# Kernel tuning notes

Hardware: AMD Instinct MI355X
Metric: run time of the kernel (lower is better)

## Reference

```python
import jax, jax.numpy as jnp
import numpy as np

HIDDEN = 512
B, H, W = 8, 48, 48
SCALE = 1.0 / np.sqrt(HIDDEN).astype(np.float32)


def conv1x1(x, w, b):
    # x: [B, C, H, W], w: [O, C], b: [O]  (1x1 Conv2d == channel matmul)
    return jnp.einsum('bchw,oc->bohw', x, w) + b[None, :, None, None]


def setup_inputs() -> dict:
    key = jax.random.key(0)
    ks = jax.random.split(key, 10)
    s = 1.0 / np.sqrt(HIDDEN)
    return {
        'locx': jax.random.normal(ks[0], (B, HIDDEN, H, W), dtype=jnp.float32),
        'glox': jax.random.normal(ks[1], (B, HIDDEN, H, W), dtype=jnp.float32),
        'Wq': jax.random.normal(ks[2], (HIDDEN, HIDDEN), dtype=jnp.float32) * s,
        'bq': jax.random.normal(ks[3], (HIDDEN,), dtype=jnp.float32) * 0.01,
        'Wk': jax.random.normal(ks[4], (HIDDEN, HIDDEN), dtype=jnp.float32) * s,
        'bk': jax.random.normal(ks[5], (HIDDEN,), dtype=jnp.float32) * 0.01,
        'Wv': jax.random.normal(ks[6], (HIDDEN, HIDDEN), dtype=jnp.float32) * s,
        'bv': jax.random.normal(ks[7], (HIDDEN,), dtype=jnp.float32) * 0.01,
        'Wo': jax.random.normal(ks[8], (HIDDEN, HIDDEN), dtype=jnp.float32) * s,
        'bo': jax.random.normal(ks[9], (HIDDEN,), dtype=jnp.float32) * 0.01,
    }


def reference(locx, glox, Wq, bq, Wk, bk, Wv, bv, Wo, bo):
    b, c, h, w = locx.shape
    # 1x1 conv projections
    q = conv1x1(locx, Wq, bq).reshape(b, c, h * w)   # [B, C, N]
    k = conv1x1(glox, Wk, bk).reshape(b, c, -1)      # [B, C, M]
    v = conv1x1(glox, Wv, bv).reshape(b, c, -1)      # [B, C, M]
    # scores = Q^T K / sqrt(hidden)  -> [B, N, M]
    scores = jnp.einsum('bcn,bcm->bnm', q, k) * SCALE
    probs = jax.nn.softmax(scores, axis=-1)           # dropout rate 0.0 -> identity
    # context = probs @ V^T -> [B, N, C] -> [B, C, H, H]
    ctx = jnp.einsum('bnm,bcm->bcn', probs, v).reshape(b, c, h, h)
    out = conv1x1(ctx, Wo, bo)                        # proj dropout 0.0 -> identity
    return out
```

## Files before the change

### kernel.cpp

```cpp
#include <hip/hip_runtime.h>
#include <hip/hip_bf16.h>

typedef __attribute__((ext_vector_type(4))) float f32x4;
typedef __attribute__((ext_vector_type(8))) short bf16x8;
typedef __attribute__((ext_vector_type(4))) short s16x4;

#define C_DIM 512
#define N_PIX 2304
#define N_BATCH 8
#define ATT_SCALE 0.04419417382415922f
#define NJB 9

typedef __attribute__((address_space(3))) unsigned int lds_u32;
typedef const __attribute__((address_space(1))) unsigned int glob_u32;

__device__ __forceinline__ void gl2lds16(const __hip_bfloat16* g, __hip_bfloat16* l)
{
    __builtin_amdgcn_global_load_lds((glob_u32*)g, (lds_u32*)l, 16, 0, 0);
}

#define GBAR() __builtin_amdgcn_s_barrier()
#define GVM0() asm volatile("s_waitcnt vmcnt(0)" ::: "memory")



#define BAR()  __builtin_amdgcn_s_barrier()
#define LGK0() asm volatile("s_waitcnt lgkmcnt(0)" ::: "memory")
#define VM4()  asm volatile("s_waitcnt vmcnt(4)" ::: "memory")
#define VM0()  asm volatile("s_waitcnt vmcnt(0)" ::: "memory")
#define PRIO(p) __builtin_amdgcn_s_setprio(p)

#define STAGE_A(dd, hh, tk) do { \
    _Pragma("unroll") \
    for (int ss = 0; ss < 2; ++ss) { \
        const int ur0 = wave * 16 + ss * 8; \
        const int row0 = ((ur0 >> 6) << 7) + (hh) * 64 + (ur0 & 63); \
        gl2lds16(gA + (size_t)row0 * C_DIM + (tk) * 64, \
                 (__hip_bfloat16*)&LA[dd][row0 * 64]); \
    } } while (0)

#define STAGE_B(dd, bb, tk) do { \
    _Pragma("unroll") \
    for (int ss = 0; ss < 2; ++ss) { \
        const int ur0 = wave * 16 + ss * 8; \
        const int row0 = ((ur0 >> 5) << 6) + (bb) * 32 + (ur0 & 31); \
        gl2lds16(gB + (size_t)row0 * C_DIM + (tk) * 64, \
                 (__hip_bfloat16*)&LB[dd][row0 * 64]); \
    } } while (0)

#define LOAD_A(dd, hh) do { \
    _Pragma("unroll") \
    for (int tt = 0; tt < 4; ++tt) { \
        const int rb = (wr * 128 + (hh) * 64 + tt * 16 + fr) * 64; \
        _Pragma("unroll") \
        for (int kk = 0; kk < 2; ++kk) \
            aF[tt][kk] = *(const bf16x8*)(&LA[dd][rb + (((kk * 4 + fq) ^ sw) << 3)]); \
    } } while (0)

#define LOAD_B(dd, bb, dst) do { \
    _Pragma("unroll") \
    for (int s2 = 0; s2 < 2; ++s2) { \
        const int rb = (wc * 64 + (bb) * 32 + s2 * 16 + fr) * 64; \
        _Pragma("unroll") \
        for (int kk = 0; kk < 2; ++kk) \
            dst[s2][kk] = *(const bf16x8*)(&LB[dd][rb + (((kk * 4 + fq) ^ sw) << 3)]); \
    } } while (0)

#define MFMA_Q(HH, BB, bsrc) do { \
    _Pragma("unroll") \
    for (int tt = 0; tt < 4; ++tt) \
    _Pragma("unroll") \
    for (int s2 = 0; s2 < 2; ++s2) \
    _Pragma("unroll") \
    for (int kk = 0; kk < 2; ++kk) \
        acc[(HH) * 4 + tt][(BB) * 2 + s2] = __builtin_amdgcn_mfma_f32_16x16x32_bf16( \
            aF[tt][kk], bsrc[s2][kk], acc[(HH) * 4 + tt][(BB) * 2 + s2], 0, 0, 0); \
    } while (0)

template<int NS>
__global__ __launch_bounds__(512, 2)
void s_only(const __hip_bfloat16* __restrict__ Tm, const __hip_bfloat16* __restrict__ Xgt,
            __hip_bfloat16* __restrict__ Pu, float* __restrict__ rp,
            const float* __restrict__ vvec, int bz_off, long sPu)
{
    __shared__ __hip_bfloat16 LA[2][256 * 64];
    __shared__ __hip_bfloat16 LB[2][256 * 64];

    const int lin = blockIdx.x;
    const int bz  = lin % NS + bz_off;
    const int t   = lin / NS;
    const int ib  = t / 9;
    const int jb  = t % 9;
    const long sQ = (long)N_PIX * C_DIM;

    const __hip_bfloat16* A = Tm  + (size_t)bz * sQ;
    const __hip_bfloat16* B = Xgt + (size_t)bz * sQ;
    __hip_bfloat16* D = Pu + (size_t)bz * (size_t)sPu;

    const int i0 = ib * 256;
    const int j0 = jb * 256;

    const int tid  = threadIdx.x;
    const int lane = tid & 63;
    const int wave = tid >> 6;

    const int lrow = lane >> 3;
    const int lcs  = (lane & 7) ^ lrow;
    const __hip_bfloat16* gA = A + (size_t)(i0 + lrow) * C_DIM + lcs * 8;
    const __hip_bfloat16* gB = B + (size_t)(j0 + lrow) * C_DIM + lcs * 8;

    const int fr = lane & 15;
    const int fq = lane >> 4;
    const int sw = fr & 7;
    const int wr = wave >> 2;
    const int wc = wave & 3;

    f32x4 acc[8][4];
#pragma unroll
    for (int a = 0; a < 8; ++a)
#pragma unroll
        for (int b = 0; b < 4; ++b)
            acc[a][b] = (f32x4){0.f, 0.f, 0.f, 0.f};

    bf16x8 aF[4][2], bF0[2][2], bF1[2][2];

    STAGE_A(0, 0, 0); STAGE_B(0, 0, 0); STAGE_B(0, 1, 0); STAGE_A(0, 1, 0);
    STAGE_A(1, 0, 1); STAGE_B(1, 1, 1);
    VM4();
    BAR();

    for (int kt = 0; kt < 6; ++kt) {
        const int d = kt & 1, e = d ^ 1;
        LOAD_A(d, 0); LOAD_B(d, 0, bF0);
        STAGE_A(e, 1, kt + 1);
        BAR(); LGK0();
        PRIO(1); MFMA_Q(0, 0, bF0); PRIO(0);
        BAR();
        LOAD_B(d, 1, bF1);
        STAGE_B(e, 0, kt + 1);
        BAR(); LGK0();
        PRIO(1); MFMA_Q(0, 1, bF1); PRIO(0);
        BAR();
        LOAD_A(d, 1);
        STAGE_A(d, 0, kt + 2);
        BAR(); LGK0();
        PRIO(1); MFMA_Q(1, 1, bF1); PRIO(0);
        BAR();
        STAGE_B(d, 1, kt + 2);
        VM4();
        BAR();
        PRIO(1); MFMA_Q(1, 0, bF0); PRIO(0);
        BAR();
    }
    {
        LOAD_A(0, 0); LOAD_B(0, 0, bF0);
        STAGE_A(1, 1, 7);
        BAR(); LGK0();
        PRIO(1); MFMA_Q(0, 0, bF0); PRIO(0);
        BAR();
        LOAD_B(0, 1, bF1);
        STAGE_B(1, 0, 7);
        BAR(); LGK0();
        PRIO(1); MFMA_Q(0, 1, bF1); PRIO(0);
        BAR();
        LOAD_A(0, 1);
        BAR(); LGK0();
        PRIO(1); MFMA_Q(1, 1, bF1); PRIO(0);
        BAR();
        VM0();
        BAR();
        PRIO(1); MFMA_Q(1, 0, bF0); PRIO(0);
        BAR();
    }
    {
        LOAD_A(1, 0); LOAD_B(1, 0, bF0);
        BAR(); LGK0();
        PRIO(1); MFMA_Q(0, 0, bF0); PRIO(0);
        BAR();
        LOAD_B(1, 1, bF1);
        BAR(); LGK0();
        PRIO(1); MFMA_Q(0, 1, bF1); PRIO(0);
        BAR();
        LOAD_A(1, 1);
        BAR(); LGK0();
        PRIO(1); MFMA_Q(1, 1, bF1); PRIO(0);
        BAR();
        PRIO(1); MFMA_Q(1, 0, bF0); PRIO(0);
    }

    float vb[4];
#pragma unroll
    for (int b = 0; b < 4; ++b)
        vb[b] = vvec[(size_t)bz * N_PIX + j0 + wc * 64 + b * 16 + fr];

    float rpart[8][4];
#pragma unroll
    for (int a = 0; a < 8; ++a)
#pragma unroll
        for (int r = 0; r < 4; ++r)
            rpart[a][r] = 0.f;
#pragma unroll
    for (int a = 0; a < 8; ++a) {
        const int grow = i0 + wr * 128 + a * 16 + fq * 4;
#pragma unroll
        for (int b = 0; b < 4; ++b) {
            const int col = j0 + wc * 64 + b * 16 + fr;
#pragma unroll
            for (int r = 0; r < 4; ++r) {
                float v = __expf(ATT_SCALE * (acc[a][b][r] + vb[b]));
                rpart[a][r] += v;
                D[(size_t)(grow + r) * N_PIX + col] = __float2bfloat16(v);
            }
        }
    }
#pragma unroll
    for (int m = 1; m < 16; m <<= 1)
#pragma unroll
        for (int a = 0; a < 8; ++a)
#pragma unroll
            for (int r = 0; r < 4; ++r)
                rpart[a][r] += __shfl_xor(rpart[a][r], m);
    float* rsl = (float*)&LA[0][0];
    __syncthreads();
    if (fr == 0) {
#pragma unroll
        for (int a = 0; a < 8; ++a)
#pragma unroll
            for (int r = 0; r < 4; ++r)
                rsl[wave * 128 + a * 16 + fq * 4 + r] = rpart[a][r];
    }
    __syncthreads();
    if (tid < 256) {
        const int wr2 = tid >> 7, rl = tid & 127;
        float s = rsl[(wr2 * 4 + 0) * 128 + rl] + rsl[(wr2 * 4 + 1) * 128 + rl]
                + rsl[(wr2 * 4 + 2) * 128 + rl] + rsl[(wr2 * 4 + 3) * 128 + rl];
        rp[((size_t)jb * N_BATCH + bz) * N_PIX + i0 + tid] = s;
    }
}

#undef STAGE_A
#undef STAGE_B
#undef LOAD_A
#undef LOAD_B
#undef MFMA_Q
#undef BAR
#undef LGK0
#undef VM4
#undef VM0
#undef PRIO


#define PV_STAGE(ee, tk) do { \
    _Pragma("unroll") \
    for (int ss = 0; ss < 2; ++ss) \
        gl2lds16(ga + (size_t)ss * 8 * N_PIX + (tk) * 64, \
                 laA + (ee) * (64 * 64) + ss * 8 * 64); \
    _Pragma("unroll") \
    for (int ss = 0; ss < 4; ++ss) \
        gl2lds16(gb + (size_t)ss * 8 * N_PIX + (tk) * 64, \
                 laB + (ee) * (128 * 64) + ss * 8 * 64); \
    } while (0)

#define PV_COMP(dd) do { \
    _Pragma("unroll") \
    for (int kk = 0; kk < 2; ++kk) { \
        bf16x8 af[2], bfr[4]; \
        const int ca = ((kk * 4 + fq) ^ sw) << 3; \
        _Pragma("unroll") \
        for (int tt = 0; tt < 2; ++tt) \
            af[tt]  = *(const bf16x8*)(&As[dd][(wi + tt * 16 + fr) * 64 + ca]); \
        _Pragma("unroll") \
        for (int tt = 0; tt < 4; ++tt) \
            bfr[tt] = *(const bf16x8*)(&Bs[dd][(wj + tt * 16 + fr) * 64 + ca]); \
        _Pragma("unroll") \
        for (int a = 0; a < 2; ++a) \
        _Pragma("unroll") \
        for (int b = 0; b < 4; ++b) \
            acc[a][b] = __builtin_amdgcn_mfma_f32_16x16x32_bf16( \
                af[a], bfr[b], acc[a][b], 0, 0, 0); \
    } } while (0)

template<int NS>
__global__ __launch_bounds__(256)
void pv_out(const __hip_bfloat16* __restrict__ Vp, const __hip_bfloat16* __restrict__ Pu,
            float* __restrict__ out, const float* __restrict__ bo,
            const float* __restrict__ rp, int bz_off, long sPu)
{
    __shared__ __hip_bfloat16 As[2][64 * 64];
    __shared__ __hip_bfloat16 Bs[2][128 * 64];

    const int lin = blockIdx.x;
    const int bz  = lin % NS + bz_off;
    const int t   = lin / NS;
    const int ib  = t % 8;
    const int jb  = t / 8;
    const int i0  = ib * 64;
    const int j0  = jb * 128;

    const long sCN = (long)C_DIM * N_PIX;
    const __hip_bfloat16* A = Vp + (size_t)bz * sCN;
    const __hip_bfloat16* B = Pu + (size_t)bz * (size_t)sPu;
    float* D = out + (size_t)bz * sCN;

    const int tid  = threadIdx.x;
    const int lane = tid & 63;
    const int wave = tid >> 6;

    const int lrow = lane >> 3;
    const int lcs  = (lane & 7) ^ lrow;
    const __hip_bfloat16* ga = A + (size_t)(i0 + wave * 16 + lrow) * N_PIX + lcs * 8;
    const __hip_bfloat16* gb = B + (size_t)(j0 + wave * 32 + lrow) * N_PIX + lcs * 8;
    __hip_bfloat16* laA = &As[0][wave * 16 * 64];
    __hip_bfloat16* laB = &Bs[0][wave * 32 * 64];

    const int fr = lane & 15;
    const int fq = lane >> 4;
    const int sw = fr & 7;
    const int wi = (wave >> 1) * 32;
    const int wj = (wave & 1) * 64;

    f32x4 acc[2][4];
#pragma unroll
    for (int a = 0; a < 2; ++a)
#pragma unroll
        for (int b = 0; b < 4; ++b)
            acc[a][b] = (f32x4){0.f, 0.f, 0.f, 0.f};

    PV_STAGE(0, 0);
    GVM0(); GBAR();

#pragma unroll 1
    for (int kt = 0; kt < 34; kt += 2) {
        PV_STAGE(1, kt + 1);
        PV_COMP(0);
        GVM0(); GBAR();
        PV_STAGE(0, kt + 2);
        PV_COMP(1);
        GVM0(); GBAR();
    }
    PV_STAGE(1, 35);
    PV_COMP(0);
    GVM0(); GBAR();
    PV_COMP(1);

    const int orow = fq * 4;
    float rjv[4];
#pragma unroll
    for (int b = 0; b < 4; ++b) {
        int j = j0 + wj + b * 16 + fr;
        float s = 0.f;
#pragma unroll
        for (int jj = 0; jj < NJB; ++jj)
            s += rp[((size_t)jj * N_BATCH + bz) * N_PIX + j];
        rjv[b] = 1.f / s;
    }

#pragma unroll
    for (int a = 0; a < 2; ++a) {
        int ibx = i0 + wi + a * 16 + orow;
#pragma unroll
        for (int r = 0; r < 4; ++r) {
            float bi = bo[ibx + r];
#pragma unroll
            for (int b = 0; b < 4; ++b) {
                int j = j0 + wj + b * 16 + fr;
                D[(size_t)(ibx + r) * N_PIX + j] = acc[a][b][r] * rjv[b] + bi;
            }
        }
    }
}

#undef PV_STAGE
#undef PV_COMP


#define PJ_STAGE(ee, tk) do { \
    _Pragma("unroll") \
    for (int ss = 0; ss < 4; ++ss) { \
        gl2lds16(ga + (size_t)ss * 8 * C_DIM + (tk) * 64, \
                 laA + (ee) * (128 * 64) + ss * 8 * 64); \
        gl2lds16(gb + (size_t)ss * 8 * C_DIM + (tk) * 64, \
                 laB + (ee) * (128 * 64) + ss * 8 * 64); \
    } } while (0)

#define PJ_COMP(dd) do { \
    _Pragma("unroll") \
    for (int kk = 0; kk < 2; ++kk) { \
        bf16x8 af[4], bfr[4]; \
        const int ca = ((kk * 4 + fq) ^ sw) << 3; \
        _Pragma("unroll") \
        for (int tt = 0; tt < 4; ++tt) { \
            af[tt]  = *(const bf16x8*)(&As[dd][(wi + tt * 16 + fr) * 64 + ca]); \
            bfr[tt] = *(const bf16x8*)(&Bs[dd][(wj + tt * 16 + fr) * 64 + ca]); \
        } \
        _Pragma("unroll") \
        for (int a = 0; a < 4; ++a) \
        _Pragma("unroll") \
        for (int b = 0; b < 4; ++b) \
            acc[a][b] = __builtin_amdgcn_mfma_f32_16x16x32_bf16( \
                af[a], bfr[b], acc[a][b], 0, 0, 0); \
    } } while (0)

#define PJ_LOOP() do { \
    PJ_STAGE(0, 0); \
    GVM0(); GBAR(); \
    _Pragma("unroll 1") \
    for (int kt = 0; kt < 6; kt += 2) { \
        PJ_STAGE(1, kt + 1); \
        PJ_COMP(0); \
        GVM0(); GBAR(); \
        PJ_STAGE(0, kt + 2); \
        PJ_COMP(1); \
        GVM0(); GBAR(); \
    } \
    PJ_STAGE(1, 7); \
    PJ_COMP(0); \
    GVM0(); GBAR(); \
    PJ_COMP(1); \
    } while (0)

__global__ __launch_bounds__(256)
void proj2(const __hip_bfloat16* __restrict__ Xlt,
           const __hip_bfloat16* __restrict__ Xgt,
           const __hip_bfloat16* __restrict__ matT,
           const __hip_bfloat16* __restrict__ Wov,
           const float* __restrict__ bovp,
           __hip_bfloat16* __restrict__ Tm,
           __hip_bfloat16* __restrict__ Vp)
{
    __shared__ __hip_bfloat16 As[2][128 * 64];
    __shared__ __hip_bfloat16 Bs[2][128 * 64];

    const int lin = blockIdx.x;
    const int s   = lin % 16;
    const int bz  = s & 7;
    const int m2  = s >> 3;
    const int t2  = lin / 16;
    const int j0  = (t2 & 3) * 128;
    const int i0  = (t2 >> 2) * 128;
    const long sNC = (long)N_PIX * C_DIM;

    const __hip_bfloat16* Ab = (m2 ? Xgt : Xlt) + (size_t)bz * sNC;
    const __hip_bfloat16* Bb = m2 ? Wov : matT;

    const int tid  = threadIdx.x;
    const int lane = tid & 63;
    const int wave = tid >> 6;

    const int lrow = lane >> 3;
    const int lcs  = (lane & 7) ^ lrow;
    const __hip_bfloat16* ga = Ab + (size_t)(i0 + wave * 32 + lrow) * C_DIM + lcs * 8;
    const __hip_bfloat16* gb = Bb + (size_t)(j0 + wave * 32 + lrow) * C_DIM + lcs * 8;
    __hip_bfloat16* laA = &As[0][wave * 32 * 64];
    __hip_bfloat16* laB = &Bs[0][wave * 32 * 64];

    const int fr = lane & 15;
    const int fq = lane >> 4;
    const int sw = fr & 7;
    const int wi = (wave >> 1) * 64;
    const int wj = (wave & 1) * 64;

    f32x4 acc[4][4];
#pragma unroll
    for (int a = 0; a < 4; ++a)
#pragma unroll
        for (int b = 0; b < 4; ++b)
            acc[a][b] = (f32x4){0.f, 0.f, 0.f, 0.f};

    PJ_LOOP();

    const int orow = fq * 4;
    if (m2 == 0) {
        __hip_bfloat16* D = Tm + (size_t)bz * sNC;
#pragma unroll
        for (int a = 0; a < 4; ++a) {
            int ibx = i0 + wi + a * 16 + orow;
#pragma unroll
            for (int b = 0; b < 4; ++b) {
                int j = j0 + wj + b * 16 + fr;
#pragma unroll
                for (int r = 0; r < 4; ++r)
                    D[(size_t)(ibx + r) * C_DIM + j] = __float2bfloat16(acc[a][b][r]);
            }
        }
    } else {
        __hip_bfloat16* Dvp = Vp + (size_t)bz * sNC;
        float bvb[4];
#pragma unroll
        for (int b = 0; b < 4; ++b)
            bvb[b] = bovp[j0 + wj + b * 16 + fr];
        __syncthreads();
        __hip_bfloat16* Tt = (__hip_bfloat16*)&As[0][0];
#pragma unroll
        for (int h = 0; h < 2; ++h) {
            if ((wave & 1) == h) {
#pragma unroll
                for (int a = 0; a < 4; ++a) {
                    int rl = wi + a * 16 + orow;
#pragma unroll
                    for (int b = 0; b < 4; ++b) {
                        int cl = b * 16 + fr;
#pragma unroll
                        for (int r = 0; r < 4; ++r)
                            Tt[(rl + r) * 65 + cl] =
                                __float2bfloat16(acc[a][b][r] + bvb[b]);
                    }
                }
            }
            __syncthreads();
            {
                const int lj = tid >> 2, ic = (tid & 3) * 32;
                union { __hip_bfloat16 h8[32]; int4 v4[4]; } u;
#pragma unroll
                for (int q = 0; q < 32; ++q)
                    u.h8[q] = Tt[(ic + q) * 65 + lj];
                __hip_bfloat16* dst = Dvp + (size_t)(j0 + h * 64 + lj) * N_PIX + i0 + ic;
#pragma unroll
                for (int q4 = 0; q4 < 4; ++q4)
                    ((int4*)dst)[q4] = u.v4[q4];
            }
            __syncthreads();
        }
    }
}

__global__ __launch_bounds__(256)
void wmix(const __hip_bfloat16* __restrict__ WkT, const __hip_bfloat16* __restrict__ WqT,
          const __hip_bfloat16* __restrict__ wo_bf, const __hip_bfloat16* __restrict__ WvT,
          __hip_bfloat16* __restrict__ matT, __hip_bfloat16* __restrict__ Wov,
          const __hip_bfloat16* __restrict__ Xgt, const float* __restrict__ wvbuf,
          float* __restrict__ vvec)
{
    __shared__ __hip_bfloat16 As[2][128 * 64];
    __shared__ __hip_bfloat16 Bs[2][128 * 64];

    const int lin = blockIdx.x;
    const int tid = threadIdx.x;

    if (lin >= 32) {
        float* wvs = (float*)&As[0][0];
        wvs[tid] = wvbuf[tid];
        wvs[tid + 256] = wvbuf[tid + 256];
        __syncthreads();
        const int blk = lin - 32;
        const int b   = blk / 9;
        const int m0  = (blk % 9) * 256;
        const __hip_bfloat16* row = Xgt + ((size_t)b * N_PIX + m0 + tid) * C_DIM;
        float acc = 0.f;
#pragma unroll 4
        for (int c8 = 0; c8 < 64; ++c8) {
            union { bf16x8 v; __hip_bfloat16 h[8]; } u;
            u.v = *(const bf16x8*)(row + c8 * 8);
#pragma unroll
            for (int j = 0; j < 8; ++j)
                acc += __bfloat162float(u.h[j]) * wvs[c8 * 8 + j];
        }
        vvec[(size_t)b * N_PIX + m0 + tid] = acc;
        return;
    }

    const int m2 = lin >> 4;
    const int t2 = lin & 15;
    const int j0 = (t2 & 3) * 128;
    const int i0 = (t2 >> 2) * 128;

    const __hip_bfloat16* Ab = m2 ? wo_bf : WkT;
    const __hip_bfloat16* Bb = m2 ? WvT   : WqT;
    __hip_bfloat16* D = m2 ? Wov : matT;

    const int lane = tid & 63;
    const int wave = tid >> 6;
    const int lrow = lane >> 3;
    const int lcs  = (lane & 7) ^ lrow;
    const __hip_bfloat16* ga = Ab + (size_t)(i0 + wave * 32 + lrow) * C_DIM + lcs * 8;
    const __hip_bfloat16* gb = Bb + (size_t)(j0 + wave * 32 + lrow) * C_DIM + lcs * 8;
    __hip_bfloat16* laA = &As[0][wave * 32 * 64];
    __hip_bfloat16* laB = &Bs[0][wave * 32 * 64];

    const int fr = lane & 15;
    const int fq = lane >> 4;
    const int sw = fr & 7;
    const int wi = (wave >> 1) * 64;
    const int wj = (wave & 1) * 64;

    f32x4 acc[4][4];
#pragma unroll
    for (int a = 0; a < 4; ++a)
#pragma unroll
        for (int b = 0; b < 4; ++b)
            acc[a][b] = (f32x4){0.f, 0.f, 0.f, 0.f};

    PJ_LOOP();

    const int orow = fq * 4;
#pragma unroll
    for (int a = 0; a < 4; ++a) {
        int ibx = i0 + wi + a * 16 + orow;
#pragma unroll
        for (int b = 0; b < 4; ++b) {
            int j = j0 + wj + b * 16 + fr;
#pragma unroll
            for (int r = 0; r < 4; ++r)
                D[(size_t)(ibx + r) * C_DIM + j] = __float2bfloat16(acc[a][b][r]);
        }
    }
}

#undef PJ_STAGE
#undef PJ_COMP
#undef PJ_LOOP

__global__ __launch_bounds__(256)
void prep(const float* __restrict__ locx, const float* __restrict__ glox,
          __hip_bfloat16* __restrict__ Xlt, __hip_bfloat16* __restrict__ Xgt,
          const float* __restrict__ Wq, const float* __restrict__ Wk,
          const float* __restrict__ Wv, const float* __restrict__ Wo,
          __hip_bfloat16* __restrict__ wo_bf,
          __hip_bfloat16* __restrict__ WqT, __hip_bfloat16* __restrict__ WkT,
          __hip_bfloat16* __restrict__ WvT,
          const float* __restrict__ bq, const float* __restrict__ bv,
          float* __restrict__ wvbuf, float* __restrict__ bovbuf)
{
    __shared__ float t[64 * 65];
    const int lin = blockIdx.x;
    const int tid = threadIdx.x;

    if (lin < 4608) {
        const int z  = lin & 15;
        const int t2 = lin >> 4;
        const int c0 = (t2 & 7) * 64;
        const int n0 = (t2 >> 3) * 64;
        const size_t b = z & 7;
        const float* Xb = ((z < 8) ? locx : glox) + b * (size_t)C_DIM * N_PIX;
        __hip_bfloat16* Xt = (z < 8) ? Xlt : Xgt;

        const int n_l = tid & 63;
        const int c_b = tid >> 6;
#pragma unroll
        for (int s = 0; s < 16; ++s) {
            int c_l = c_b + s * 4;
            t[c_l * 65 + n_l] = Xb[(size_t)(c0 + c_l) * N_PIX + n0 + n_l];
        }
        __syncthreads();

        const int cc = (tid & 7) * 8;
        const int nb = tid >> 3;
#pragma unroll
        for (int it = 0; it < 2; ++it) {
            int n2 = nb + it * 32;
            union { __hip_bfloat16 h[8]; int4 v; } u;
#pragma unroll
            for (int w = 0; w < 8; ++w)
                u.h[w] = __float2bfloat16(t[(cc + w) * 65 + n2]);
            *(int4*)(&Xt[(b * N_PIX + n0 + n2) * C_DIM + c0 + cc]) = u.v;
        }
    } else if (lin < 4864) {
        const int idx = lin - 4608;
        const int i = (idx * 256 + tid) * 4;
        float4 f = *(const float4*)(Wo + i);
        union { __hip_bfloat16 h[4]; s16x4 q; } u;
        u.h[0] = __float2bfloat16(f.x);
        u.h[1] = __float2bfloat16(f.y);
        u.h[2] = __float2bfloat16(f.z);
        u.h[3] = __float2bfloat16(f.w);
        *(s16x4*)(wo_bf + i) = u.q;
    } else if (lin < 5056) {
        const int widx = lin - 4864;
        const int w    = widx >> 6;
        const int tile = widx & 63;
        const float* S = (w == 0) ? Wq : (w == 1) ? Wk : Wv;
        __hip_bfloat16* Dt = (w == 0) ? WqT : (w == 1) ? WkT : WvT;
        const int o0  = (tile & 7) * 64;
        const int c0t = (tile >> 3) * 64;

        const int n_l = tid & 63;
        const int c_b = tid >> 6;
#pragma unroll
        for (int s = 0; s < 16; ++s) {
            int o_l = c_b + s * 4;
            t[o_l * 65 + n_l] = S[(size_t)(o0 + o_l) * 512 + c0t + n_l];
        }
        __syncthreads();

        const int cc = (tid & 7) * 8;
        const int nb = tid >> 3;
#pragma unroll
        for (int it = 0; it < 2; ++it) {
            int c_r = nb + it * 32;
            union { __hip_bfloat16 h[8]; int4 v; } u;
#pragma unroll
            for (int w8 = 0; w8 < 8; ++w8)
                u.h[w8] = __float2bfloat16(t[(cc + w8) * 65 + c_r]);
            *(int4*)(&Dt[(size_t)(c0t + c_r) * 512 + o0 + cc]) = u.v;
        }
    } else if (lin == 5056) {
        float a0 = 0.f, a1 = 0.f;
        for (int o = 0; o < 512; ++o) {
            float bb = bq[o];
            a0 += Wk[(size_t)o * 512 + tid] * bb;
            a1 += Wk[(size_t)o * 512 + tid + 256] * bb;
        }
        wvbuf[tid] = a0;
        wvbuf[tid + 256] = a1;
    } else {
#pragma unroll
        for (int half = 0; half < 2; ++half) {
            int o = tid + half * 256;
            float acc = 0.f;
            for (int c4 = 0; c4 < 128; ++c4) {
                float4 f = *(const float4*)(Wo + (size_t)o * 512 + c4 * 4);
                float4 g = *(const float4*)(bv + c4 * 4);
                acc += f.x * g.x + f.y * g.y + f.z * g.z + f.w * g.w;
            }
            bovbuf[o] = acc;
        }
    }
}

extern "C" void kernel_launch(void* const* d_in, const int* in_sizes, int n_in,
                              void* d_out, int out_size, void* d_ws, size_t ws_size,
                              hipStream_t stream)
{
    const float* locx = (const float*)d_in[0];
    const float* glox = (const float*)d_in[1];
    const float* Wq = (const float*)d_in[2];
    const float* bq = (const float*)d_in[3];
    const float* Wk = (const float*)d_in[4];
    const float* bk = (const float*)d_in[5];
    const float* Wv = (const float*)d_in[6];
    const float* bv = (const float*)d_in[7];
    const float* Wo = (const float*)d_in[8];
    const float* bo = (const float*)d_in[9];
    float* out = (float*)d_out;
    (void)bk;

    const int C = C_DIM, N = N_PIX;
    const size_t WB   = (size_t)C * C * 2;
    const size_t szX  = (size_t)N_BATCH * N * C * 2;
    const size_t szP1 = (size_t)N * N * 2;
    const size_t szRP = (size_t)NJB * N_BATCH * N * 4;
    const size_t szV  = (size_t)N_BATCH * N * 4;

    char* ws = (char*)d_ws;
    size_t off = 0;
    auto alloc = [&](size_t bytes) {
        char* p = ws + off;
        off += (bytes + 255) & ~(size_t)255;
        return p;
    };
    __hip_bfloat16* wo_bf = (__hip_bfloat16*)alloc(WB);
    __hip_bfloat16* WqT   = (__hip_bfloat16*)alloc(WB);
    __hip_bfloat16* WkT   = (__hip_bfloat16*)alloc(WB);
    __hip_bfloat16* WvT   = (__hip_bfloat16*)alloc(WB);
    __hip_bfloat16* matT  = (__hip_bfloat16*)alloc(WB);
    __hip_bfloat16* Wov   = (__hip_bfloat16*)alloc(WB);
    float*          wvb   = (float*)alloc(512 * 4);
    float*          bovb  = (float*)alloc(512 * 4);
    float*          vvec  = (float*)alloc(szV);
    __hip_bfloat16* Xlt   = (__hip_bfloat16*)alloc(szX);
    __hip_bfloat16* Xgt   = (__hip_bfloat16*)alloc(szX);
    __hip_bfloat16* Tm    = (__hip_bfloat16*)alloc(szX);
    __hip_bfloat16* Vp    = (__hip_bfloat16*)alloc(szX);
    float*          rp    = (float*)alloc(szRP);
    const size_t fixed = off;
    bool full = (ws_size >= fixed + 8 * szP1 + 4096);
    __hip_bfloat16* Pu = (__hip_bfloat16*)alloc(full ? 8 * szP1 : szP1);

    const dim3 blk(256);

    prep<<<dim3(5058), blk, 0, stream>>>(locx, glox, Xlt, Xgt,
                                         Wq, Wk, Wv, Wo, wo_bf, WqT, WkT, WvT,
                                         bq, bv, wvb, bovb);
    wmix<<<dim3(104), blk, 0, stream>>>(WkT, WqT, wo_bf, WvT, matT, Wov,
                                        Xgt, wvb, vvec);
    proj2<<<dim3(16 * 72), blk, 0, stream>>>(Xlt, Xgt, matT, Wov, bovb, Tm, Vp);

    if (full) {
        s_only<8><<<dim3(8 * 81), dim3(512), 0, stream>>>(
            Tm, Xgt, Pu, rp, vvec, 0, (long)N * N);
        pv_out<8><<<dim3(8 * 144), blk, 0, stream>>>(
            Vp, Pu, out, bo, rp, 0, (long)N * N);
    } else {
        for (int r = 0; r < N_BATCH; ++r) {
            s_only<1><<<dim3(81), dim3(512), 0, stream>>>(
                Tm, Xgt, Pu, rp, vvec, r, 0);
            pv_out<1><<<dim3(144), blk, 0, stream>>>(
                Vp, Pu, out, bo, rp, r, 0);
        }
    }
}
```

Measured before the change: 359.9 us.

## Merge weight prep into single kernel and enlarge PV output tile to 128x128

The separate weight-transpose/convert pass and the wmix kernel are folded into one prep kernel. It computes the Wk^T·Wq and Wo·Wv mixes directly from fp32 weights converted on the fly into LDS, and computes vvec directly from glox. This removes one launch and the intermediate bf16 transposed weight buffers. Separately, pv_out's tile grows from 64x128 to 128x128 with 4x4 MFMA accumulators per wave, which halves the block count and the redundant reloads of the P matrix, at the cost of more registers and LDS per block.

```diff
diff --git a/kernel.cpp b/kernel.cpp
--- a/kernel.cpp
+++ b/kernel.cpp
@@ -252,28 +252,25 @@
 
 #define PV_STAGE(ee, tk) do { \
     _Pragma("unroll") \
-    for (int ss = 0; ss < 2; ++ss) \
+    for (int ss = 0; ss < 4; ++ss) { \
         gl2lds16(ga + (size_t)ss * 8 * N_PIX + (tk) * 64, \
-                 laA + (ee) * (64 * 64) + ss * 8 * 64); \
-    _Pragma("unroll") \
-    for (int ss = 0; ss < 4; ++ss) \
+                 laA + (ee) * (128 * 64) + ss * 8 * 64); \
         gl2lds16(gb + (size_t)ss * 8 * N_PIX + (tk) * 64, \
                  laB + (ee) * (128 * 64) + ss * 8 * 64); \
-    } while (0)
+    } } while (0)
 
 #define PV_COMP(dd) do { \
     _Pragma("unroll") \
     for (int kk = 0; kk < 2; ++kk) { \
-        bf16x8 af[2], bfr[4]; \
+        bf16x8 af[4], bfr[4]; \
         const int ca = ((kk * 4 + fq) ^ sw) << 3; \
         _Pragma("unroll") \
-        for (int tt = 0; tt < 2; ++tt) \
+        for (int tt = 0; tt < 4; ++tt) { \
             af[tt]  = *(const bf16x8*)(&As[dd][(wi + tt * 16 + fr) * 64 + ca]); \
+            bfr[tt] = *(const bf16x8*)(&Bs[dd][(wj + tt * 16 + fr) * 64 + ca]); \
+        } \
         _Pragma("unroll") \
-        for (int tt = 0; tt < 4; ++tt) \
-            bfr[tt] = *(const bf16x8*)(&Bs[dd][(wj + tt * 16 + fr) * 64 + ca]); \
-        _Pragma("unroll") \
-        for (int a = 0; a < 2; ++a) \
+        for (int a = 0; a < 4; ++a) \
         _Pragma("unroll") \
         for (int b = 0; b < 4; ++b) \
             acc[a][b] = __builtin_amdgcn_mfma_f32_16x16x32_bf16( \
@@ -286,15 +283,15 @@
             float* __restrict__ out, const float* __restrict__ bo,
             const float* __restrict__ rp, int bz_off, long sPu)
 {
-    __shared__ __hip_bfloat16 As[2][64 * 64];
+    __shared__ __hip_bfloat16 As[2][128 * 64];
     __shared__ __hip_bfloat16 Bs[2][128 * 64];
 
     const int lin = blockIdx.x;
     const int bz  = lin % NS + bz_off;
     const int t   = lin / NS;
-    const int ib  = t % 8;
-    const int jb  = t / 8;
-    const int i0  = ib * 64;
+    const int ib  = t % 4;
+    const int jb  = t / 4;
+    const int i0  = ib * 128;
     const int j0  = jb * 128;
 
     const long sCN = (long)C_DIM * N_PIX;
@@ -308,20 +305,20 @@
 
     const int lrow = lane >> 3;
     const int lcs  = (lane & 7) ^ lrow;
-    const __hip_bfloat16* ga = A + (size_t)(i0 + wave * 16 + lrow) * N_PIX + lcs * 8;
+    const __hip_bfloat16* ga = A + (size_t)(i0 + wave * 32 + lrow) * N_PIX + lcs * 8;
     const __hip_bfloat16* gb = B + (size_t)(j0 + wave * 32 + lrow) * N_PIX + lcs * 8;
-    __hip_bfloat16* laA = &As[0][wave * 16 * 64];
+    __hip_bfloat16* laA = &As[0][wave * 32 * 64];
     __hip_bfloat16* laB = &Bs[0][wave * 32 * 64];
 
     const int fr = lane & 15;
     const int fq = lane >> 4;
     const int sw = fr & 7;
-    const int wi = (wave >> 1) * 32;
+    const int wi = (wave >> 1) * 64;
     const int wj = (wave & 1) * 64;
 
-    f32x4 acc[2][4];
-#pragma unroll
-    for (int a = 0; a < 2; ++a)
+    f32x4 acc[4][4];
+#pragma unroll
+    for (int a = 0; a < 4; ++a)
 #pragma unroll
         for (int b = 0; b < 4; ++b)
             acc[a][b] = (f32x4){0.f, 0.f, 0.f, 0.f};
@@ -356,7 +353,7 @@
     }
 
 #pragma unroll
-    for (int a = 0; a < 2; ++a) {
+    for (int a = 0; a < 4; ++a) {
         int ibx = i0 + wi + a * 16 + orow;
 #pragma unroll
         for (int r = 0; r < 4; ++r) {
@@ -524,185 +521,151 @@
     }
 }
 
+#undef PJ_STAGE
+#undef PJ_COMP
+#undef PJ_LOOP
+
 __global__ __launch_bounds__(256)
-void wmix(const __hip_bfloat16* __restrict__ WkT, const __hip_bfloat16* __restrict__ WqT,
-          const __hip_bfloat16* __restrict__ wo_bf, const __hip_bfloat16* __restrict__ WvT,
+void prep(const float* __restrict__ locx, const float* __restrict__ glox,
+          const float* __restrict__ Wq, const float* __restrict__ Wk,
+          const float* __restrict__ Wv, const float* __restrict__ Wo,
+          const float* __restrict__ bq, const float* __restrict__ bv,
+          __hip_bfloat16* __restrict__ Xlt, __hip_bfloat16* __restrict__ Xgt,
           __hip_bfloat16* __restrict__ matT, __hip_bfloat16* __restrict__ Wov,
-          const __hip_bfloat16* __restrict__ Xgt, const float* __restrict__ wvbuf,
-          float* __restrict__ vvec)
+          float* __restrict__ vvec, float* __restrict__ bovbuf)
 {
-    __shared__ __hip_bfloat16 As[2][128 * 64];
-    __shared__ __hip_bfloat16 Bs[2][128 * 64];
-
+    __shared__ __align__(16) char shm[16640];
     const int lin = blockIdx.x;
     const int tid = threadIdx.x;
 
-    if (lin >= 32) {
-        float* wvs = (float*)&As[0][0];
-        wvs[tid] = wvbuf[tid];
-        wvs[tid + 256] = wvbuf[tid + 256];
-        __syncthreads();
+    if (lin < 32) {
+        __hip_bfloat16* As = (__hip_bfloat16*)shm;
+        __hip_bfloat16* Bs = (__hip_bfloat16*)(shm + 8192);
+        const int m2 = lin >> 4;
+        const int t2 = lin & 15;
+        const int j0 = (t2 & 3) * 128;
+        const int i0 = (t2 >> 2) * 128;
+
+        const int lane = tid & 63;
+        const int wave = tid >> 6;
+        const int fr = lane & 15;
+        const int fq = lane >> 4;
+        const int sw2 = fr & 3;
+        const int wi = (wave >> 1) * 64;
+        const int wj = (wave & 1) * 64;
+
+        f32x4 acc[4][4];
+#pragma unroll
+        for (int a = 0; a < 4; ++a)
+#pragma unroll
+            for (int b = 0; b < 4; ++b)
+                acc[a][b] = (f32x4){0.f, 0.f, 0.f, 0.f};
+
+        const float* SB = m2 ? Wv : Wq;
+        const int o_r = tid >> 3;
+        const int cc0 = (tid & 7) * 16;
+
+#pragma unroll 1
+        for (int o0 = 0; o0 < 512; o0 += 32) {
+            if (m2 == 0) {
+                const float* src = Wk + (size_t)(o0 + o_r) * 512 + i0 + cc0;
+                float v[16];
+#pragma unroll
+                for (int q4 = 0; q4 < 4; ++q4) {
+                    float4 f = *(const float4*)(src + q4 * 4);
+                    v[q4 * 4 + 0] = f.x; v[q4 * 4 + 1] = f.y;
+                    v[q4 * 4 + 2] = f.z; v[q4 * 4 + 3] = f.w;
+                }
+#pragma unroll
+                for (int q = 0; q < 16; ++q) {
+                    const int col = cc0 + q;
+                    const int byt = col * 64 + ((((o_r >> 3) ^ (col & 3)) << 4))
+                                  + (o_r & 7) * 2;
+                    *(__hip_bfloat16*)((char*)As + byt) = __float2bfloat16(v[q]);
+                }
+            } else {
+                const int r = tid >> 1;
+#pragma unroll
+                for (int s = 0; s < 2; ++s) {
+                    const int cp = (tid & 1) * 2 + s;
+                    const float* src = Wo + (size_t)(i0 + r) * 512 + o0 + cp * 8;
+                    float4 f0 = *(const float4*)(src);
+                    float4 f1 = *(const float4*)(src + 4);
+                    union { __hip_bfloat16 h[8]; int4 v4; } u;
+                    u.h[0] = __float2bfloat16(f0.x); u.h[1] = __float2bfloat16(f0.y);
+                    u.h[2] = __float2bfloat16(f0.z); u.h[3] = __float2bfloat16(f0.w);
+                    u.h[4] = __float2bfloat16(f1.x); u.h[5] = __float2bfloat16(f1.y);
+                    u.h[6] = __float2bfloat16(f1.z); u.h[7] = __float2bfloat16(f1.w);
+                    *(int4*)(As + r * 32 + ((cp ^ (r & 3)) << 3)) = u.v4;
+                }
+            }
+            {
+                const float* src = SB + (size_t)(o0 + o_r) * 512 + j0 + cc0;
+                float v[16];
+#pragma unroll
+                for (int q4 = 0; q4 < 4; ++q4) {
+                    float4 f = *(const float4*)(src + q4 * 4);
+                    v[q4 * 4 + 0] = f.x; v[q4 * 4 + 1] = f.y;
+                    v[q4 * 4 + 2] = f.z; v[q4 * 4 + 3] = f.w;
+                }
+#pragma unroll
+                for (int q = 0; q < 16; ++q) {
+                    const int col = cc0 + q;
+                    const int byt = col * 64 + ((((o_r >> 3) ^ (col & 3)) << 4))
+                                  + (o_r & 7) * 2;
+                    *(__hip_bfloat16*)((char*)Bs + byt) = __float2bfloat16(v[q]);
+                }
+            }
+            __syncthreads();
+            bf16x8 af[4], bfm[4];
+#pragma unroll
+            for (int tt = 0; tt < 4; ++tt) {
+                af[tt]  = *(const bf16x8*)(As + (wi + tt * 16 + fr) * 32
+                                              + ((fq ^ sw2) << 3));
+                bfm[tt] = *(const bf16x8*)(Bs + (wj + tt * 16 + fr) * 32
+                                              + ((fq ^ sw2) << 3));
+            }
+#pragma unroll
+            for (int a = 0; a < 4; ++a)
+#pragma unroll
+                for (int b = 0; b < 4; ++b)
+                    acc[a][b] = __builtin_amdgcn_mfma_f32_16x16x32_bf16(
+                        af[a], bfm[b], acc[a][b], 0, 0, 0);
+            __syncthreads();
+        }
+        __hip_bfloat16* D = m2 ? Wov : matT;
+        const int orow = fq * 4;
+#pragma unroll
+        for (int a = 0; a < 4; ++a) {
+            int ibx = i0 + wi + a * 16 + orow;
+#pragma unroll
+            for (int b = 0; b < 4; ++b) {
+                int j = j0 + wj + b * 16 + fr;
+#pragma unroll
+                for (int r = 0; r < 4; ++r)
+                    D[(size_t)(ibx + r) * 512 + j] = __float2bfloat16(acc[a][b][r]);
+            }
+        }
+    } else if (lin < 104) {
         const int blk = lin - 32;
         const int b   = blk / 9;
         const int m0  = (blk % 9) * 256;
-        const __hip_bfloat16* row = Xgt + ((size_t)b * N_PIX + m0 + tid) * C_DIM;
-        float acc = 0.f;
-#pragma unroll 4
-        for (int c8 = 0; c8 < 64; ++c8) {
-            union { bf16x8 v; __hip_bfloat16 h[8]; } u;
-            u.v = *(const bf16x8*)(row + c8 * 8);
-#pragma unroll
-            for (int j = 0; j < 8; ++j)
-                acc += __bfloat162float(u.h[j]) * wvs[c8 * 8 + j];
-        }
-        vvec[(size_t)b * N_PIX + m0 + tid] = acc;
-        return;
-    }
-
-    const int m2 = lin >> 4;
-    const int t2 = lin & 15;
-    const int j0 = (t2 & 3) * 128;
-    const int i0 = (t2 >> 2) * 128;
-
-    const __hip_bfloat16* Ab = m2 ? wo_bf : WkT;
-    const __hip_bfloat16* Bb = m2 ? WvT   : WqT;
-    __hip_bfloat16* D = m2 ? Wov : matT;
-
-    const int lane = tid & 63;
-    const int wave = tid >> 6;
-    const int lrow = lane >> 3;
-    const int lcs  = (lane & 7) ^ lrow;
-    const __hip_bfloat16* ga = Ab + (size_t)(i0 + wave * 32 + lrow) * C_DIM + lcs * 8;
-    const __hip_bfloat16* gb = Bb + (size_t)(j0 + wave * 32 + lrow) * C_DIM + lcs * 8;
-    __hip_bfloat16* laA = &As[0][wave * 32 * 64];
-    __hip_bfloat16* laB = &Bs[0][wave * 32 * 64];
-
-    const int fr = lane & 15;
-    const int fq = lane >> 4;
-    const int sw = fr & 7;
-    const int wi = (wave >> 1) * 64;
-    const int wj = (wave & 1) * 64;
-
-    f32x4 acc[4][4];
-#pragma unroll
-    for (int a = 0; a < 4; ++a)
-#pragma unroll
-        for (int b = 0; b < 4; ++b)
-            acc[a][b] = (f32x4){0.f, 0.f, 0.f, 0.f};
-
-    PJ_LOOP();
-
-    const int orow = fq * 4;
-#pragma unroll
-    for (int a = 0; a < 4; ++a) {
-        int ibx = i0 + wi + a * 16 + orow;
-#pragma unroll
-        for (int b = 0; b < 4; ++b) {
-            int j = j0 + wj + b * 16 + fr;
-#pragma unroll
-            for (int r = 0; r < 4; ++r)
-                D[(size_t)(ibx + r) * C_DIM + j] = __float2bfloat16(acc[a][b][r]);
-        }
-    }
-}
-
-#undef PJ_STAGE
-#undef PJ_COMP
-#undef PJ_LOOP
-
-__global__ __launch_bounds__(256)
-void prep(const float* __restrict__ locx, const float* __restrict__ glox,
-          __hip_bfloat16* __restrict__ Xlt, __hip_bfloat16* __restrict__ Xgt,
-          const float* __restrict__ Wq, const float* __restrict__ Wk,
-          const float* __restrict__ Wv, const float* __restrict__ Wo,
-          __hip_bfloat16* __restrict__ wo_bf,
-          __hip_bfloat16* __restrict__ WqT, __hip_bfloat16* __restrict__ WkT,
-          __hip_bfloat16* __restrict__ WvT,
-          const float* __restrict__ bq, const float* __restrict__ bv,
-          float* __restrict__ wvbuf, float* __restrict__ bovbuf)
-{
-    __shared__ float t[64 * 65];
-    const int lin = blockIdx.x;
-    const int tid = threadIdx.x;
-
-    if (lin < 4608) {
-        const int z  = lin & 15;
-        const int t2 = lin >> 4;
-        const int c0 = (t2 & 7) * 64;
-        const int n0 = (t2 >> 3) * 64;
-        const size_t b = z & 7;
-        const float* Xb = ((z < 8) ? locx : glox) + b * (size_t)C_DIM * N_PIX;
-        __hip_bfloat16* Xt = (z < 8) ? Xlt : Xgt;
-
-        const int n_l = tid & 63;
-        const int c_b = tid >> 6;
-#pragma unroll
-        for (int s = 0; s < 16; ++s) {
-            int c_l = c_b + s * 4;
-            t[c_l * 65 + n_l] = Xb[(size_t)(c0 + c_l) * N_PIX + n0 + n_l];
-        }
-        __syncthreads();
-
-        const int cc = (tid & 7) * 8;
-        const int nb = tid >> 3;
-#pragma unroll
-        for (int it = 0; it < 2; ++it) {
-            int n2 = nb + it * 32;
-            union { __hip_bfloat16 h[8]; int4 v; } u;
-#pragma unroll
-            for (int w = 0; w < 8; ++w)
-                u.h[w] = __float2bfloat16(t[(cc + w) * 65 + n2]);
-            *(int4*)(&Xt[(b * N_PIX + n0 + n2) * C_DIM + c0 + cc]) = u.v;
-        }
-    } else if (lin < 4864) {
-        const int idx = lin - 4608;
-        const int i = (idx * 256 + tid) * 4;
-        float4 f = *(const float4*)(Wo + i);
-        union { __hip_bfloat16 h[4]; s16x4 q; } u;
-        u.h[0] = __float2bfloat16(f.x);
-        u.h[1] = __float2bfloat16(f.y);
-        u.h[2] = __float2bfloat16(f.z);
-        u.h[3] = __float2bfloat16(f.w);
-        *(s16x4*)(wo_bf + i) = u.q;
-    } else if (lin < 5056) {
-        const int widx = lin - 4864;
-        const int w    = widx >> 6;
-        const int tile = widx & 63;
-        const float* S = (w == 0) ? Wq : (w == 1) ? Wk : Wv;
-        __hip_bfloat16* Dt = (w == 0) ? WqT : (w == 1) ? WkT : WvT;
-        const int o0  = (tile & 7) * 64;
-        const int c0t = (tile >> 3) * 64;
-
-        const int n_l = tid & 63;
-        const int c_b = tid >> 6;
-#pragma unroll
-        for (int s = 0; s < 16; ++s) {
-            int o_l = c_b + s * 4;
-            t[o_l * 65 + n_l] = S[(size_t)(o0 + o_l) * 512 + c0t + n_l];
-        }
-        __syncthreads();
-
-        const int cc = (tid & 7) * 8;
-        const int nb = tid >> 3;
-#pragma unroll
-        for (int it = 0; it < 2; ++it) {
-            int c_r = nb + it * 32;
-            union { __hip_bfloat16 h[8]; int4 v; } u;
-#pragma unroll
-            for (int w8 = 0; w8 < 8; ++w8)
-                u.h[w8] = __float2bfloat16(t[(cc + w8) * 65 + c_r]);
-            *(int4*)(&Dt[(size_t)(c0t + c_r) * 512 + o0 + cc]) = u.v;
-        }
-    } else if (lin == 5056) {
         float a0 = 0.f, a1 = 0.f;
         for (int o = 0; o < 512; ++o) {
-            float bb = bq[o];
+            const float bb = bq[o];
             a0 += Wk[(size_t)o * 512 + tid] * bb;
             a1 += Wk[(size_t)o * 512 + tid + 256] * bb;
         }
-        wvbuf[tid] = a0;
-        wvbuf[tid + 256] = a1;
-    } else {
+        float* wvs = (float*)shm;
+        wvs[tid] = a0;
+        wvs[tid + 256] = a1;
+        __syncthreads();
+        const float* col = glox + (size_t)b * 512 * N_PIX + m0 + tid;
+        float acc = 0.f;
+        for (int c = 0; c < 512; ++c)
+            acc += col[(size_t)c * N_PIX] * wvs[c];
+        vvec[(size_t)b * N_PIX + m0 + tid] = acc;
+    } else if (lin == 104) {
 #pragma unroll
         for (int half = 0; half < 2; ++half) {
             int o = tid + half * 256;
@@ -713,6 +676,37 @@
                 acc += f.x * g.x + f.y * g.y + f.z * g.z + f.w * g.w;
             }
             bovbuf[o] = acc;
+        }
+    } else {
+        float* t = (float*)shm;
+        const int lin2 = lin - 105;
+        const int z  = lin2 & 15;
+        const int t2 = lin2 >> 4;
+        const int c0 = (t2 & 7) * 64;
+        const int n0 = (t2 >> 3) * 64;
+        const size_t b = z & 7;
+        const float* Xb = ((z < 8) ? locx : glox) + b * (size_t)C_DIM * N_PIX;
+        __hip_bfloat16* Xt = (z < 8) ? Xlt : Xgt;
+
+        const int n_l = tid & 63;
+        const int c_b = tid >> 6;
+#pragma unroll
+        for (int s = 0; s < 16; ++s) {
+            int c_l = c_b + s * 4;
+            t[c_l * 65 + n_l] = Xb[(size_t)(c0 + c_l) * N_PIX + n0 + n_l];
+        }
+        __syncthreads();
+
+        const int cc = (tid & 7) * 8;
+        const int nb = tid >> 3;
+#pragma unroll
+        for (int it = 0; it < 2; ++it) {
+            int n2 = nb + it * 32;
+            union { __hip_bfloat16 h[8]; int4 v; } u;
+#pragma unroll
+            for (int w = 0; w < 8; ++w)
+                u.h[w] = __float2bfloat16(t[(cc + w) * 65 + n2]);
+            *(int4*)(&Xt[(b * N_PIX + n0 + n2) * C_DIM + c0 + cc]) = u.v;
         }
     }
 }
@@ -748,13 +742,8 @@
         off += (bytes + 255) & ~(size_t)255;
         return p;
     };
-    __hip_bfloat16* wo_bf = (__hip_bfloat16*)alloc(WB);
-    __hip_bfloat16* WqT   = (__hip_bfloat16*)alloc(WB);
-    __hip_bfloat16* WkT   = (__hip_bfloat16*)alloc(WB);
-    __hip_bfloat16* WvT   = (__hip_bfloat16*)alloc(WB);
     __hip_bfloat16* matT  = (__hip_bfloat16*)alloc(WB);
     __hip_bfloat16* Wov   = (__hip_bfloat16*)alloc(WB);
-    float*          wvb   = (float*)alloc(512 * 4);
     float*          bovb  = (float*)alloc(512 * 4);
     float*          vvec  = (float*)alloc(szV);
     __hip_bfloat16* Xlt   = (__hip_bfloat16*)alloc(szX);
@@ -768,23 +757,20 @@
 
     const dim3 blk(256);
 
-    prep<<<dim3(5058), blk, 0, stream>>>(locx, glox, Xlt, Xgt,
-                                         Wq, Wk, Wv, Wo, wo_bf, WqT, WkT, WvT,
-                                         bq, bv, wvb, bovb);
-    wmix<<<dim3(104), blk, 0, stream>>>(WkT, WqT, wo_bf, WvT, matT, Wov,
-                                        Xgt, wvb, vvec);
+    prep<<<dim3(4713), blk, 0, stream>>>(locx, glox, Wq, Wk, Wv, Wo, bq, bv,
+                                         Xlt, Xgt, matT, Wov, vvec, bovb);
     proj2<<<dim3(16 * 72), blk, 0, stream>>>(Xlt, Xgt, matT, Wov, bovb, Tm, Vp);
 
     if (full) {
         s_only<8><<<dim3(8 * 81), dim3(512), 0, stream>>>(
             Tm, Xgt, Pu, rp, vvec, 0, (long)N * N);
-        pv_out<8><<<dim3(8 * 144), blk, 0, stream>>>(
+        pv_out<8><<<dim3(8 * 72), blk, 0, stream>>>(
             Vp, Pu, out, bo, rp, 0, (long)N * N);
     } else {
         for (int r = 0; r < N_BATCH; ++r) {
             s_only<1><<<dim3(81), dim3(512), 0, stream>>>(
                 Tm, Xgt, Pu, rp, vvec, r, 0);
-            pv_out<1><<<dim3(144), blk, 0, stream>>>(
+            pv_out<1><<<dim3(72), blk, 0, stream>>>(
                 Vp, Pu, out, bo, rp, r, 0);
         }
     }
```

After: 366.2 us. No clear change (+1.7%).
